# Optimization experiments

Hardware: AMD Instinct MI355X
Metric: run time of the kernel (lower is better)

The kernel has to match this reference:

```python
import jax, jax.numpy as jnp
import numpy as np

N_NODES = 100000


def _gcn_conv(x, src, dst, W, b, n_nodes):
    # PyG GCNConv: out = D^{-1/2} (A + I) D^{-1/2} (x W) + b
    h = x @ W  # [N, out]
    # degree including self-loop
    ones = jnp.ones(src.shape[0], dtype=h.dtype)
    deg = jax.ops.segment_sum(ones, dst, num_segments=n_nodes) + 1.0
    dinv = jax.lax.rsqrt(deg)  # [N]
    # neighbor messages: gather from src, normalize, scatter-add to dst
    norm = dinv[src] * dinv[dst]  # [E]
    msg = h[src] * norm[:, None]  # [E, out]
    agg = jax.ops.segment_sum(msg, dst, num_segments=n_nodes)
    # self-loop contribution: norm_ii = dinv[i]^2
    agg = agg + h * (dinv * dinv)[:, None]
    return agg + b


def setup_inputs() -> dict:
    key = jax.random.key(0)
    ks = jax.random.split(key, 10)
    x = jax.random.normal(ks[0], (N_NODES, 64), dtype=jnp.float32)
    edge_index = jax.random.randint(ks[1], (2, 1000000), 0, N_NODES, dtype=jnp.int64)
    def glorot(k, shape):
        lim = np.sqrt(6.0 / (shape[0] + shape[1]))
        return jax.random.uniform(k, shape, jnp.float32, -lim, lim)
    return {
        "x": x,
        "edge_index": edge_index,
        "W1": glorot(ks[2], (64, 80)), "b1": jnp.zeros((80,), jnp.float32),
        "W2": glorot(ks[3], (80, 40)), "b2": jnp.zeros((40,), jnp.float32),
        "W3": glorot(ks[4], (40, 50)), "b3": jnp.zeros((50,), jnp.float32),
        "Wl": glorot(ks[5], (50, 10)), "bl": jnp.zeros((10,), jnp.float32),
    }


def reference(x, edge_index, W1, b1, W2, b2, W3, b3, Wl, bl):
    src, dst = edge_index[0], edge_index[1]
    n = x.shape[0]
    h = _gcn_conv(x, src, dst, W1, b1, n)
    h = jax.nn.leaky_relu(h, negative_slope=0.01)
    # dropout is identity in eval mode
    h = _gcn_conv(h, src, dst, W2, b2, n)
    h = jax.nn.leaky_relu(h, negative_slope=0.01)
    h = _gcn_conv(h, src, dst, W3, b3, n)
    h = jax.nn.leaky_relu(h, negative_slope=0.01)
    logits = h @ Wl + bl
    return jax.nn.log_softmax(logits, axis=1)
```

## Files before the change

### kernel.cpp

```cpp
#include <hip/hip_runtime.h>

#define LEAKY(v) ((v) > 0.0f ? (v) : 0.01f * (v))
#define NBUK_MAX 512

__device__ __forceinline__ unsigned short f2bf(float f) {
    unsigned u = __float_as_uint(f);
    u += 0x7fffu + ((u >> 16) & 1u);
    return (unsigned short)(u >> 16);
}
__device__ __forceinline__ unsigned pack2bf(float lo, float hi) {
    return (unsigned)f2bf(lo) | ((unsigned)f2bf(hi) << 16);
}
__device__ __forceinline__ float4 bf4_to_f4(uint2 u) {
    float4 r;
    r.x = __uint_as_float(u.x << 16);
    r.y = __uint_as_float(u.x & 0xffff0000u);
    r.z = __uint_as_float(u.y << 16);
    r.w = __uint_as_float(u.y & 0xffff0000u);
    return r;
}

__device__ __forceinline__ int detect_is64(const unsigned* ei, int E) {
    __shared__ int is64_s;
    if (threadIdx.x == 0) {
        int z = 1;
        int limit = 2 * E < 128 ? 2 * E : 128;
        for (int i = 1; i < limit; i += 2)
            if (ei[i] != 0u) { z = 0; break; }
        is64_s = z;
    }
    __syncthreads();
    return is64_s;
}

__global__ __launch_bounds__(256) void bucket_count_kernel(
    const unsigned* __restrict__ ei, int* __restrict__ s32, int* __restrict__ d32,
    int* __restrict__ gcount, int E, int nblk, int nbuk, int ch) {
    __shared__ int hist[NBUK_MAX];
    int is64 = detect_is64(ei, E);
    for (int i = threadIdx.x; i < nbuk; i += 256) hist[i] = 0;
    __syncthreads();
    int base = blockIdx.x * ch;
    int lim = min(base + ch, E);
    for (int e = base + threadIdx.x; e < lim; e += 256) {
        int s, d;
        if (is64) {
            s = (int)ei[2 * (size_t)e];
            d = (int)ei[2 * (size_t)E + 2 * (size_t)e];
        } else {
            s = (int)ei[e];
            d = (int)ei[(size_t)E + e];
        }
        s32[e] = s;
        d32[e] = d;
        atomicAdd(&hist[d >> 8], 1);
    }
    __syncthreads();
    for (int i = threadIdx.x; i < nbuk; i += 256)
        gcount[(size_t)i * nblk + blockIdx.x] = hist[i];
}

__global__ __launch_bounds__(256) void bucket_total_kernel(
    const int* __restrict__ gcount, int* __restrict__ btot, int nblk) {
    __shared__ int s[256];
    int sum = 0;
    for (int i = threadIdx.x; i < nblk; i += 256)
        sum += gcount[(size_t)blockIdx.x * nblk + i];
    s[threadIdx.x] = sum;
    __syncthreads();
    for (int off = 128; off > 0; off >>= 1) {
        if (threadIdx.x < off) s[threadIdx.x] += s[threadIdx.x + off];
        __syncthreads();
    }
    if (threadIdx.x == 0) btot[blockIdx.x] = s[0];
}

__global__ __launch_bounds__(512) void scan_btot_kernel(
    const int* __restrict__ btot, int* __restrict__ bbase,
    int* __restrict__ row_ofs, int nbuk, int N, int E) {
    __shared__ int s[512];
    int t = threadIdx.x;
    int v = (t < nbuk) ? btot[t] : 0;
    s[t] = v;
    __syncthreads();
    for (int off = 1; off < 512; off <<= 1) {
        int add = (t >= off) ? s[t - off] : 0;
        __syncthreads();
        s[t] += add;
        __syncthreads();
    }
    if (t < nbuk) bbase[t] = s[t] - v;
    if (t == 0) { bbase[nbuk] = E; row_ofs[N] = E; }
}

__global__ __launch_bounds__(256) void scan_gcount_kernel(
    int* __restrict__ gcount, const int* __restrict__ bbase, int nblk) {
    __shared__ int s[256];
    int t = threadIdx.x;
    int v = (t < nblk) ? gcount[(size_t)blockIdx.x * nblk + t] : 0;
    s[t] = v;
    __syncthreads();
    for (int off = 1; off < 256; off <<= 1) {
        int add = (t >= off) ? s[t - off] : 0;
        __syncthreads();
        s[t] += add;
        __syncthreads();
    }
    if (t < nblk)
        gcount[(size_t)blockIdx.x * nblk + t] = bbase[blockIdx.x] + s[t] - v;
}

__global__ __launch_bounds__(256) void bucket_scatter_kernel(
    const int* __restrict__ s32, const int* __restrict__ d32,
    const int* __restrict__ gofs, unsigned* __restrict__ es_tmp,
    int E, int nblk, int nbuk, int ch) {
    __shared__ int cur[NBUK_MAX];
    for (int i = threadIdx.x; i < nbuk; i += 256)
        cur[i] = gofs[(size_t)i * nblk + blockIdx.x];
    __syncthreads();
    int base = blockIdx.x * ch;
    int lim = min(base + ch, E);
    for (int e = base + threadIdx.x; e < lim; e += 256) {
        int s = s32[e], d = d32[e];
        int p = atomicAdd(&cur[d >> 8], 1);
        es_tmp[p] = ((unsigned)(d & 255) << 24) | (unsigned)s;
    }
}

__global__ __launch_bounds__(256) void bucket_sortcvt_kernel(
    const unsigned* __restrict__ es_tmp, const int* __restrict__ bbase,
    int* __restrict__ es, int* __restrict__ row_ofs, float* __restrict__ dinv,
    const float* __restrict__ x, ushort4* __restrict__ xb, int N) {
    __shared__ int hist[256];
    __shared__ int lofs[256];
    __shared__ float sdinv[256];
    int b = blockIdx.x;
    int t = threadIdx.x;
    int beg = bbase[b], end = bbase[b + 1];
    hist[t] = 0;
    __syncthreads();
    for (int j = beg + t; j < end; j += 256)
        atomicAdd(&hist[es_tmp[j] >> 24], 1);
    __syncthreads();
    int v = hist[t];
    lofs[t] = v;
    __syncthreads();
    for (int off = 1; off < 256; off <<= 1) {
        int add = (t >= off) ? lofs[t - off] : 0;
        __syncthreads();
        lofs[t] += add;
        __syncthreads();
    }
    int excl = lofs[t] - v;
    int node = (b << 8) + t;
    float dv = rsqrtf((float)v + 1.0f);
    if (node <= N) row_ofs[node] = beg + excl;
    if (node < N) dinv[node] = dv;
    sdinv[t] = dv;
    __syncthreads();
    lofs[t] = beg + excl;
    __syncthreads();
    for (int j = beg + t; j < end; j += 256) {
        unsigned ed = es_tmp[j];
        int p = atomicAdd(&lofs[ed >> 24], 1);
        es[p] = (int)(ed & 0xFFFFFFu);
    }
    int qbase = (b << 8) * 16;
    for (int q = t; q < 256 * 16; q += 256) {
        int nl = q >> 4;
        int n = (b << 8) + nl;
        if (n >= N) break;
        float dn = sdinv[nl];
        float4 vv = ((const float4*)x)[qbase + q];
        ushort4 o;
        o.x = f2bf(vv.x * dn); o.y = f2bf(vv.y * dn);
        o.z = f2bf(vv.z * dn); o.w = f2bf(vv.w * dn);
        xb[qbase + q] = o;
    }
}

__global__ __launch_bounds__(256) void gather64_bf16_kernel(
    const unsigned short* __restrict__ hb, const int* __restrict__ es,
    const int* __restrict__ row_ofs, const float* __restrict__ dinv,
    unsigned short* __restrict__ agg, int N) {
    int wid = (blockIdx.x * blockDim.x + threadIdx.x) >> 6;
    int lane = threadIdx.x & 63;
    int g = lane >> 3, l = lane & 7;
    int node = wid * 8 + g;
    bool active = node < N;
    int beg = 0, end = 0;
    float dd = 0.f;
    if (active) {
        beg = row_ofs[node];
        end = row_ofs[node + 1];
        dd = dinv[node];
    }
    float4 aL = make_float4(0.f, 0.f, 0.f, 0.f);
    float4 aH = make_float4(0.f, 0.f, 0.f, 0.f);
    int j = beg;
    for (; j + 2 <= end; j += 2) {
        int s0 = es[j], s1 = es[j + 1];
        uint4 h0 = *(const uint4*)&hb[(size_t)s0 * 64 + 8 * l];
        uint4 h1 = *(const uint4*)&hb[(size_t)s1 * 64 + 8 * l];
        float4 l0 = bf4_to_f4(make_uint2(h0.x, h0.y));
        float4 i0 = bf4_to_f4(make_uint2(h0.z, h0.w));
        float4 l1 = bf4_to_f4(make_uint2(h1.x, h1.y));
        float4 i1 = bf4_to_f4(make_uint2(h1.z, h1.w));
        aL.x += l0.x + l1.x; aL.y += l0.y + l1.y;
        aL.z += l0.z + l1.z; aL.w += l0.w + l1.w;
        aH.x += i0.x + i1.x; aH.y += i0.y + i1.y;
        aH.z += i0.z + i1.z; aH.w += i0.w + i1.w;
    }
    if (j < end) {
        int s0 = es[j];
        uint4 h0 = *(const uint4*)&hb[(size_t)s0 * 64 + 8 * l];
        float4 l0 = bf4_to_f4(make_uint2(h0.x, h0.y));
        float4 i0 = bf4_to_f4(make_uint2(h0.z, h0.w));
        aL.x += l0.x; aL.y += l0.y; aL.z += l0.z; aL.w += l0.w;
        aH.x += i0.x; aH.y += i0.y; aH.z += i0.z; aH.w += i0.w;
    }
    if (active) {
        uint4 sr = *(const uint4*)&hb[(size_t)node * 64 + 8 * l];
        float4 sL = bf4_to_f4(make_uint2(sr.x, sr.y));
        float4 sH = bf4_to_f4(make_uint2(sr.z, sr.w));
        uint4 o;
        o.x = pack2bf((aL.x + sL.x) * dd, (aL.y + sL.y) * dd);
        o.y = pack2bf((aL.z + sL.z) * dd, (aL.w + sL.w) * dd);
        o.z = pack2bf((aH.x + sH.x) * dd, (aH.y + sH.y) * dd);
        o.w = pack2bf((aH.z + sH.z) * dd, (aH.w + sH.w) * dd);
        *(uint4*)&agg[(size_t)node * 64 + 8 * l] = o;
    }
}

template <bool BIAS, bool PRESCALE_LEAKY>
__global__ __launch_bounds__(256) void gather40_bf16_kernel(
    const unsigned short* __restrict__ hb, const int* __restrict__ es,
    const int* __restrict__ row_ofs, const float* __restrict__ dinv,
    const float* __restrict__ b, unsigned short* __restrict__ agg, int N) {
    int wid = (blockIdx.x * blockDim.x + threadIdx.x) >> 6;
    int lane = threadIdx.x & 63;
    int g = lane / 5;
    int l = lane - g * 5;
    int node = wid * 12 + g;
    bool active = (g < 12) && (node < N);
    int beg = 0, end = 0;
    float dd = 0.f;
    if (active) {
        beg = row_ofs[node];
        end = row_ofs[node + 1];
        dd = dinv[node];
    }
    float4 aL = make_float4(0.f, 0.f, 0.f, 0.f);
    float4 aH = make_float4(0.f, 0.f, 0.f, 0.f);
    int j = beg;
    for (; j + 2 <= end; j += 2) {
        int s0 = es[j], s1 = es[j + 1];
        uint4 h0 = *(const uint4*)&hb[(size_t)s0 * 40 + 8 * l];
        uint4 h1 = *(const uint4*)&hb[(size_t)s1 * 40 + 8 * l];
        float4 l0 = bf4_to_f4(make_uint2(h0.x, h0.y));
        float4 i0 = bf4_to_f4(make_uint2(h0.z, h0.w));
        float4 l1 = bf4_to_f4(make_uint2(h1.x, h1.y));
        float4 i1 = bf4_to_f4(make_uint2(h1.z, h1.w));
        aL.x += l0.x + l1.x; aL.y += l0.y + l1.y;
        aL.z += l0.z + l1.z; aL.w += l0.w + l1.w;
        aH.x += i0.x + i1.x; aH.y += i0.y + i1.y;
        aH.z += i0.z + i1.z; aH.w += i0.w + i1.w;
    }
    if (j < end) {
        int s0 = es[j];
        uint4 h0 = *(const uint4*)&hb[(size_t)s0 * 40 + 8 * l];
        float4 l0 = bf4_to_f4(make_uint2(h0.x, h0.y));
        float4 i0 = bf4_to_f4(make_uint2(h0.z, h0.w));
        aL.x += l0.x; aL.y += l0.y; aL.z += l0.z; aL.w += l0.w;
        aH.x += i0.x; aH.y += i0.y; aH.z += i0.z; aH.w += i0.w;
    }
    if (active) {
        uint4 sr = *(const uint4*)&hb[(size_t)node * 40 + 8 * l];
        float4 sL = bf4_to_f4(make_uint2(sr.x, sr.y));
        float4 sH = bf4_to_f4(make_uint2(sr.z, sr.w));
        float r0 = (aL.x + sL.x) * dd, r1 = (aL.y + sL.y) * dd;
        float r2 = (aL.z + sL.z) * dd, r3 = (aL.w + sL.w) * dd;
        float r4 = (aH.x + sH.x) * dd, r5 = (aH.y + sH.y) * dd;
        float r6 = (aH.z + sH.z) * dd, r7 = (aH.w + sH.w) * dd;
        if (BIAS) {
            float4 b0 = *(const float4*)&b[8 * l];
            float4 b1 = *(const float4*)&b[8 * l + 4];
            r0 += b0.x; r1 += b0.y; r2 += b0.z; r3 += b0.w;
            r4 += b1.x; r5 += b1.y; r6 += b1.z; r7 += b1.w;
        }
        if (PRESCALE_LEAKY) {
            r0 = LEAKY(r0) * dd; r1 = LEAKY(r1) * dd;
            r2 = LEAKY(r2) * dd; r3 = LEAKY(r3) * dd;
            r4 = LEAKY(r4) * dd; r5 = LEAKY(r5) * dd;
            r6 = LEAKY(r6) * dd; r7 = LEAKY(r7) * dd;
        }
        uint4 o;
        o.x = pack2bf(r0, r1); o.y = pack2bf(r2, r3);
        o.z = pack2bf(r4, r5); o.w = pack2bf(r6, r7);
        *(uint4*)&agg[(size_t)node * 40 + 8 * l] = o;
    }
}

template <int K, int M, bool ACT, bool BIAS, bool SCALE>
__global__ __launch_bounds__(256) void gemm_tiled_bf16(
    const unsigned short* __restrict__ x, const float* __restrict__ W,
    const float* __restrict__ b, const float* __restrict__ dinv,
    unsigned short* __restrict__ hv, int N) {
    constexpr int MT = 4;
    constexpr int MC = (M + MT - 1) / MT;
    constexpr int MP = MC * MT;
    constexpr int NR = 256 / MC;
    constexpr int NT = 4;
    constexpr int BN = NR * NT;
    static_assert(K % 4 == 0 && M % 4 == 0, "K,M multiples of 4");

    __shared__ float ws[K * MP];
    for (int i = threadIdx.x; i < K * MP; i += 256) {
        int k = i / MP, m = i - k * MP;
        ws[i] = (m < M) ? W[k * M + m] : 0.0f;
    }
    __syncthreads();

    const int c = threadIdx.x % MC;
    const int r = threadIdx.x / MC;
    if (r >= NR) return;
    const int n0 = blockIdx.x * BN + r * NT;

    float acc[NT][MT];
#pragma unroll
    for (int i = 0; i < NT; ++i)
#pragma unroll
        for (int j = 0; j < MT; ++j) {
            int m = c * MT + j;
            acc[i][j] = (BIAS && m < M) ? b[m] : 0.0f;
        }

    for (int k = 0; k < K; k += 4) {
        float4 wv[4];
#pragma unroll
        for (int kk = 0; kk < 4; ++kk)
            wv[kk] = *(const float4*)&ws[(k + kk) * MP + c * MT];
#pragma unroll
        for (int i = 0; i < NT; ++i) {
            int n = n0 + i;
            if (n < N) {
                float4 xv = bf4_to_f4(*(const uint2*)&x[(size_t)n * K + k]);
                if (ACT) {
                    xv.x = LEAKY(xv.x); xv.y = LEAKY(xv.y);
                    xv.z = LEAKY(xv.z); xv.w = LEAKY(xv.w);
                }
                const float xs[4] = {xv.x, xv.y, xv.z, xv.w};
#pragma unroll
                for (int kk = 0; kk < 4; ++kk) {
                    const float* wp = (const float*)&wv[kk];
#pragma unroll
                    for (int j = 0; j < MT; ++j)
                        acc[i][j] = fmaf(xs[kk], wp[j], acc[i][j]);
                }
            }
        }
    }

#pragma unroll
    for (int i = 0; i < NT; ++i) {
        int n = n0 + i;
        if (n >= N) continue;
        float sc = SCALE ? dinv[n] : 1.0f;
        int m = c * MT;
        ushort4 o;
        o.x = f2bf(acc[i][0] * sc); o.y = f2bf(acc[i][1] * sc);
        o.z = f2bf(acc[i][2] * sc); o.w = f2bf(acc[i][3] * sc);
        *(ushort4*)&hv[(size_t)n * M + m] = o;
    }
}

__global__ __launch_bounds__(256) void l3head_kernel(
    const unsigned short* __restrict__ P, const float* __restrict__ W3,
    const float* __restrict__ b3, const float* __restrict__ Wl,
    const float* __restrict__ bl, float* __restrict__ out, int N) {
    __shared__ float w3s[40 * 50];
    __shared__ float b3s[50];
    __shared__ float wls[50 * 10];
    __shared__ float bls[10];
    for (int i = threadIdx.x; i < 2000; i += 256) w3s[i] = W3[i];
    for (int i = threadIdx.x; i < 500; i += 256) wls[i] = Wl[i];
    if (threadIdx.x < 50) b3s[threadIdx.x] = b3[threadIdx.x];
    if (threadIdx.x < 10) bls[threadIdx.x] = bl[threadIdx.x];
    __syncthreads();
    int n = blockIdx.x * blockDim.x + threadIdx.x;
    if (n >= N) return;

    float p[40];
    const uint2* pr = (const uint2*)(P + (size_t)n * 40);
#pragma unroll
    for (int q = 0; q < 10; ++q) {
        float4 t = bf4_to_f4(pr[q]);
        p[4 * q + 0] = t.x; p[4 * q + 1] = t.y; p[4 * q + 2] = t.z; p[4 * q + 3] = t.w;
    }
    float logits[10];
#pragma unroll
    for (int j = 0; j < 10; ++j) logits[j] = bls[j];
    for (int m = 0; m < 50; ++m) {
        float acc = b3s[m];
#pragma unroll
        for (int k = 0; k < 40; ++k) acc = fmaf(p[k], w3s[k * 50 + m], acc);
        float v = LEAKY(acc);
#pragma unroll
        for (int j = 0; j < 10; ++j) logits[j] = fmaf(v, wls[m * 10 + j], logits[j]);
    }
    float mx = logits[0];
#pragma unroll
    for (int j = 1; j < 10; ++j) mx = fmaxf(mx, logits[j]);
    float s = 0.0f;
#pragma unroll
    for (int j = 0; j < 10; ++j) s += __expf(logits[j] - mx);
    float lse = __logf(s) + mx;
    float* op = out + (size_t)n * 10;
#pragma unroll
    for (int j = 0; j < 10; ++j) op[j] = logits[j] - lse;
}

extern "C" void kernel_launch(void* const* d_in, const int* in_sizes, int n_in,
                              void* d_out, int out_size, void* d_ws, size_t ws_size,
                              hipStream_t stream) {
    const float* x  = (const float*)d_in[0];
    const unsigned* ei = (const unsigned*)d_in[1];
    const float* W1 = (const float*)d_in[2];
    const float* b1 = (const float*)d_in[3];
    const float* W2 = (const float*)d_in[4];
    const float* b2 = (const float*)d_in[5];
    const float* W3 = (const float*)d_in[6];
    const float* b3 = (const float*)d_in[7];
    const float* Wl = (const float*)d_in[8];
    const float* bl = (const float*)d_in[9];
    float* out = (float*)d_out;

    const int N = in_sizes[0] / 64;
    const int E = in_sizes[1] / 2;

    int ch = 4096;
    int nblk = (E + ch - 1) / ch;
    if (nblk > 256) { ch = (E + 255) / 256; nblk = (E + ch - 1) / ch; }
    const int nbuk = (N + 255) >> 8;

    char* wp = (char*)d_ws;
    auto alloc = [&](size_t bytes) {
        char* p = wp;
        wp += (bytes + 255) & ~(size_t)255;
        return p;
    };
    int*   es      = (int*)alloc((size_t)E * 4);
    float* dinv    = (float*)alloc((size_t)N * 4);
    int*   row_ofs = (int*)alloc((size_t)(N + 1) * 4);
    int*   gcount  = (int*)alloc((size_t)nbuk * nblk * 4);
    int*   btot    = (int*)alloc((size_t)NBUK_MAX * 4);
    int*   bbase   = (int*)alloc((size_t)(NBUK_MAX + 1) * 4);
    char*  Pr      = (char*)alloc((size_t)N * 64 * 4);
    char*  Ar      = (char*)alloc((size_t)N * 80 * 4);

    int*      s32    = (int*)Pr;
    int*      d32    = (int*)Pr + E;
    unsigned* es_tmp = (unsigned*)Ar;
    size_t xb_off = (((size_t)E * 4) + 255) & ~(size_t)255;
    unsigned short* xb = (unsigned short*)(Ar + xb_off);
    unsigned short* Pg = (unsigned short*)Pr;
    unsigned short* A  = (unsigned short*)Ar;
    unsigned short* Pb = (unsigned short*)Pr;
    unsigned short* Ab = (unsigned short*)(Ar + (size_t)N * 80 * 4 - (size_t)N * 40 * 2);
    unsigned short* P3 = (unsigned short*)Pr;

    const int B = 256;

    bucket_count_kernel<<<nblk, B, 0, stream>>>(ei, s32, d32, gcount, E, nblk, nbuk, ch);
    bucket_total_kernel<<<nbuk, B, 0, stream>>>(gcount, btot, nblk);
    scan_btot_kernel<<<1, 512, 0, stream>>>(btot, bbase, row_ofs, nbuk, N, E);
    scan_gcount_kernel<<<nbuk, B, 0, stream>>>(gcount, bbase, nblk);
    bucket_scatter_kernel<<<nblk, B, 0, stream>>>(s32, d32, gcount, es_tmp, E, nblk, nbuk, ch);
    bucket_sortcvt_kernel<<<nbuk, B, 0, stream>>>(es_tmp, bbase, es, row_ofs, dinv,
                                                  x, (ushort4*)xb, N);

    const int blk64 = ((N + 7) / 8 + 3) / 4;
    const int blk40 = ((N + 11) / 12 + 3) / 4;

    auto gb = [&](int M) {
        int MC = (M + 3) / 4;
        int BN = (256 / MC) * 4;
        return (N + BN - 1) / BN;
    };

    gather64_bf16_kernel<<<blk64, B, 0, stream>>>(xb, es, row_ofs, dinv, Pg, N);
    gemm_tiled_bf16<64, 80, false, true, false><<<gb(80), B, 0, stream>>>(Pg, W1, b1, nullptr, A, N);

    gemm_tiled_bf16<80, 40, true, false, true><<<gb(40), B, 0, stream>>>(A, W2, nullptr, dinv, Pb, N);
    gather40_bf16_kernel<true, true><<<blk40, B, 0, stream>>>(Pb, es, row_ofs, dinv, b2, Ab, N);

    gather40_bf16_kernel<false, false><<<blk40, B, 0, stream>>>(Ab, es, row_ofs, dinv, nullptr, P3, N);
    l3head_kernel<<<(N + B - 1) / B, B, 0, stream>>>(P3, W3, b3, Wl, bl, out, N);
}
```

Baseline: 301.1 us.

## Replace scalar tiled GEMMs with MFMA bf16 GEMMs using split-precision weights

Swaps the two FMA-based tiled GEMM kernels for kernels that use the 16x16x32 bf16 MFMA instruction, one wave per 16-row tile. A new prep kernel packs W1 and W2 into MFMA fragment layout as a hi/lo bf16 pair, so weight precision is kept near fp32. The leaky ReLU moves from the second GEMM's input load to the first GEMM's output. The intent is to cut ALU-bound GEMM time, at the cost of an extra small launch, scalar per-element bf16 stores, and a swizzled LDS layout.

Result: faster. 267.0 us (-11.3%).

```diff
diff --git a/kernel.cpp b/kernel.cpp
--- a/kernel.cpp
+++ b/kernel.cpp
@@ -2,6 +2,9 @@
 
 #define LEAKY(v) ((v) > 0.0f ? (v) : 0.01f * (v))
 #define NBUK_MAX 512
+
+typedef __attribute__((ext_vector_type(8))) short bf16x8;
+typedef __attribute__((ext_vector_type(4))) float f32x4;
 
 __device__ __forceinline__ unsigned short f2bf(float f) {
     unsigned u = __float_as_uint(f);
@@ -301,76 +304,93 @@
     }
 }
 
-template <int K, int M, bool ACT, bool BIAS, bool SCALE>
-__global__ __launch_bounds__(256) void gemm_tiled_bf16(
-    const unsigned short* __restrict__ x, const float* __restrict__ W,
-    const float* __restrict__ b, const float* __restrict__ dinv,
-    unsigned short* __restrict__ hv, int N) {
-    constexpr int MT = 4;
-    constexpr int MC = (M + MT - 1) / MT;
-    constexpr int MP = MC * MT;
-    constexpr int NR = 256 / MC;
-    constexpr int NT = 4;
-    constexpr int BN = NR * NT;
-    static_assert(K % 4 == 0 && M % 4 == 0, "K,M multiples of 4");
-
-    __shared__ float ws[K * MP];
-    for (int i = threadIdx.x; i < K * MP; i += 256) {
-        int k = i / MP, m = i - k * MP;
-        ws[i] = (m < M) ? W[k * M + m] : 0.0f;
-    }
-    __syncthreads();
-
-    const int c = threadIdx.x % MC;
-    const int r = threadIdx.x / MC;
-    if (r >= NR) return;
-    const int n0 = blockIdx.x * BN + r * NT;
-
-    float acc[NT][MT];
-#pragma unroll
-    for (int i = 0; i < NT; ++i)
-#pragma unroll
-        for (int j = 0; j < MT; ++j) {
-            int m = c * MT + j;
-            acc[i][j] = (BIAS && m < M) ? b[m] : 0.0f;
+__global__ __launch_bounds__(256) void prep_wfrags_kernel(
+    const float* __restrict__ W1, const float* __restrict__ W2,
+    unsigned short* __restrict__ wfrag) {
+    int t = blockIdx.x * 256 + threadIdx.x;
+    if (t >= 2432) return;
+    const float* W;
+    int u, NKC, M, K;
+    if (t < 1280) { u = t; W = W1; NKC = 2; M = 80; K = 64; }
+    else          { u = t - 1280; W = W2; NKC = 3; M = 40; K = 80; }
+    int f = u >> 6, lane = u & 63;
+    int s = f & 1, mtkc = f >> 1;
+    int kc = mtkc % NKC, mt = mtkc / NKC;
+    int col = mt * 16 + (lane & 15);
+#pragma unroll
+    for (int j = 0; j < 8; ++j) {
+        int k = kc * 32 + ((lane >> 4) << 3) + j;
+        float w = (k < K && col < M) ? W[k * M + col] : 0.0f;
+        unsigned short hi = f2bf(w);
+        unsigned short v = s ? f2bf(w - __uint_as_float((unsigned)hi << 16)) : hi;
+        wfrag[(size_t)t * 8 + j] = v;
+    }
+}
+
+template <int KBF, int M, int NKC, int NMT, bool LEAKY_OUT, bool BIAS, bool SCALE>
+__global__ __launch_bounds__(256) void gemm_mfma_bf16(
+    const unsigned short* __restrict__ X, const unsigned short* __restrict__ wfrag,
+    const float* __restrict__ bvec, const float* __restrict__ dinv,
+    unsigned short* __restrict__ out, int N) {
+    static_assert(KBF <= NKC * 32 && M <= NMT * 16, "tile coverage");
+    constexpr int NFR = NMT * NKC * 2;
+    __shared__ bf16x8 wlds[NFR * 64];
+    for (int i = threadIdx.x; i < NFR * 64; i += 256) {
+        int f = i >> 6, ln = i & 63;
+        wlds[f * 64 + (ln ^ (ln >> 3))] = *(const bf16x8*)&wfrag[(size_t)i * 8];
+    }
+    __syncthreads();
+    int wid = blockIdx.x * 4 + (threadIdx.x >> 6);
+    int ntiles = (N + 15) >> 4;
+    if (wid >= ntiles) return;
+    int lane = threadIdx.x & 63;
+    int kid = lane >> 4;
+    int lidx = lane ^ (lane >> 3);
+    int base = wid * 16;
+    int arow = base + (lane & 15);
+    if (arow >= N) arow = N - 1;
+
+    bf16x8 a[NKC];
+#pragma unroll
+    for (int kc = 0; kc < NKC; ++kc) {
+        int k0 = kc * 32 + kid * 8;
+        if (k0 < KBF)
+            a[kc] = *(const bf16x8*)&X[(size_t)arow * KBF + k0];
+        else
+            a[kc] = (bf16x8){0, 0, 0, 0, 0, 0, 0, 0};
+    }
+    f32x4 acc[NMT];
+#pragma unroll
+    for (int mt = 0; mt < NMT; ++mt) acc[mt] = (f32x4){0.f, 0.f, 0.f, 0.f};
+#pragma unroll
+    for (int mt = 0; mt < NMT; ++mt) {
+#pragma unroll
+        for (int kc = 0; kc < NKC; ++kc) {
+            acc[mt] = __builtin_amdgcn_mfma_f32_16x16x32_bf16(
+                a[kc], wlds[((mt * NKC + kc) * 2 + 0) * 64 + lidx], acc[mt], 0, 0, 0);
+            acc[mt] = __builtin_amdgcn_mfma_f32_16x16x32_bf16(
+                a[kc], wlds[((mt * NKC + kc) * 2 + 1) * 64 + lidx], acc[mt], 0, 0, 0);
         }
-
-    for (int k = 0; k < K; k += 4) {
-        float4 wv[4];
-#pragma unroll
-        for (int kk = 0; kk < 4; ++kk)
-            wv[kk] = *(const float4*)&ws[(k + kk) * MP + c * MT];
-#pragma unroll
-        for (int i = 0; i < NT; ++i) {
-            int n = n0 + i;
-            if (n < N) {
-                float4 xv = bf4_to_f4(*(const uint2*)&x[(size_t)n * K + k]);
-                if (ACT) {
-                    xv.x = LEAKY(xv.x); xv.y = LEAKY(xv.y);
-                    xv.z = LEAKY(xv.z); xv.w = LEAKY(xv.w);
-                }
-                const float xs[4] = {xv.x, xv.y, xv.z, xv.w};
-#pragma unroll
-                for (int kk = 0; kk < 4; ++kk) {
-                    const float* wp = (const float*)&wv[kk];
-#pragma unroll
-                    for (int j = 0; j < MT; ++j)
-                        acc[i][j] = fmaf(xs[kk], wp[j], acc[i][j]);
-                }
+    }
+    float dv[4];
+#pragma unroll
+    for (int r = 0; r < 4; ++r)
+        dv[r] = SCALE ? dinv[min(base + kid * 4 + r, N - 1)] : 1.0f;
+#pragma unroll
+    for (int mt = 0; mt < NMT; ++mt) {
+        int col = mt * 16 + (lane & 15);
+        if (col >= M) continue;
+        float bb = BIAS ? bvec[col] : 0.0f;
+#pragma unroll
+        for (int r = 0; r < 4; ++r) {
+            int orow = base + kid * 4 + r;
+            if (orow < N) {
+                float v = acc[mt][r] + bb;
+                if (LEAKY_OUT) v = LEAKY(v);
+                if (SCALE) v *= dv[r];
+                out[(size_t)orow * M + col] = f2bf(v);
             }
         }
-    }
-
-#pragma unroll
-    for (int i = 0; i < NT; ++i) {
-        int n = n0 + i;
-        if (n >= N) continue;
-        float sc = SCALE ? dinv[n] : 1.0f;
-        int m = c * MT;
-        ushort4 o;
-        o.x = f2bf(acc[i][0] * sc); o.y = f2bf(acc[i][1] * sc);
-        o.z = f2bf(acc[i][2] * sc); o.w = f2bf(acc[i][3] * sc);
-        *(ushort4*)&hv[(size_t)n * M + m] = o;
     }
 }
 
@@ -455,6 +475,7 @@
     int*   gcount  = (int*)alloc((size_t)nbuk * nblk * 4);
     int*   btot    = (int*)alloc((size_t)NBUK_MAX * 4);
     int*   bbase   = (int*)alloc((size_t)(NBUK_MAX + 1) * 4);
+    unsigned short* wfrag = (unsigned short*)alloc((size_t)2432 * 8 * 2);
     char*  Pr      = (char*)alloc((size_t)N * 64 * 4);
     char*  Ar      = (char*)alloc((size_t)N * 80 * 4);
 
@@ -471,6 +492,8 @@
 
     const int B = 256;
 
+    prep_wfrags_kernel<<<10, B, 0, stream>>>(W1, W2, wfrag);
+
     bucket_count_kernel<<<nblk, B, 0, stream>>>(ei, s32, d32, gcount, E, nblk, nbuk, ch);
     bucket_total_kernel<<<nbuk, B, 0, stream>>>(gcount, btot, nblk);
     scan_btot_kernel<<<1, 512, 0, stream>>>(btot, bbase, row_ofs, nbuk, N, E);
@@ -482,16 +505,15 @@
     const int blk64 = ((N + 7) / 8 + 3) / 4;
     const int blk40 = ((N + 11) / 12 + 3) / 4;
 
-    auto gb = [&](int M) {
-        int MC = (M + 3) / 4;
-        int BN = (256 / MC) * 4;
-        return (N + BN - 1) / BN;
-    };
+    const int ntiles = (N + 15) / 16;
+    const int gemm_blocks = (ntiles + 3) / 4;
 
     gather64_bf16_kernel<<<blk64, B, 0, stream>>>(xb, es, row_ofs, dinv, Pg, N);
-    gemm_tiled_bf16<64, 80, false, true, false><<<gb(80), B, 0, stream>>>(Pg, W1, b1, nullptr, A, N);
-
-    gemm_tiled_bf16<80, 40, true, false, true><<<gb(40), B, 0, stream>>>(A, W2, nullptr, dinv, Pb, N);
+    gemm_mfma_bf16<64, 80, 2, 5, true, true, false>
+        <<<gemm_blocks, B, 0, stream>>>(Pg, wfrag, b1, nullptr, A, N);
+
+    gemm_mfma_bf16<80, 40, 3, 3, false, false, true>
+        <<<gemm_blocks, B, 0, stream>>>(A, wfrag + 20 * 512, nullptr, dinv, Pb, N);
     gather40_bf16_kernel<true, true><<<blk40, B, 0, stream>>>(Pb, es, row_ofs, dinv, b2, Ab, N);
 
     gather40_bf16_kernel<false, false><<<blk40, B, 0, stream>>>(Ab, es, row_ofs, dinv, nullptr, P3, N);
```
